# Optimization experiments

Hardware: AMD Instinct MI355X
Metric: run time of the kernel (lower is better)

Reference implementation:

```python
import jax, jax.numpy as jnp
import numpy as np

D_MODEL = 1024
N_HEADS = 16
D_HEAD = D_MODEL // N_HEADS
D_FF = 4096
THETA = 10000.0
EPS = 1e-5


def rmsnorm(x, g):
    xf = x.astype(jnp.float32)
    rms = jnp.sqrt(jnp.mean(xf * xf, axis=-1, keepdims=True) + EPS)
    return ((xf / rms) * g).astype(x.dtype)


def rope(x, pos):
    # x: (B, H, S, d_head); pos: (S,) int
    dk = x.shape[-1]
    inv_freq = 1.0 / (THETA ** (jnp.arange(0, dk, 2, dtype=jnp.float32) / dk))
    freqs = pos.astype(jnp.float32)[:, None] * inv_freq[None, :]  # (S, dk/2)
    cos, sin = jnp.cos(freqs), jnp.sin(freqs)
    xp = x.reshape(*x.shape[:-1], dk // 2, 2)
    xe, xo = xp[..., 0], xp[..., 1]
    re = xe * cos - xo * sin
    ro = xe * sin + xo * cos
    return jnp.stack([re, ro], axis=-1).reshape(x.shape)


def attention(x, pos, q_w, k_w, v_w, o_w):
    B, S, D = x.shape
    def heads(t):
        return t.reshape(B, S, N_HEADS, D_HEAD).transpose(0, 2, 1, 3)
    Q = heads(x @ q_w.T)
    K = heads(x @ k_w.T)
    V = heads(x @ v_w.T)
    Q = rope(Q, pos)
    K = rope(K, pos)
    scores = jnp.einsum('bhqd,bhkd->bhqk', Q, K) / jnp.sqrt(jnp.float32(D_HEAD))
    causal = jnp.tril(jnp.ones((S, S), dtype=bool))
    scores = jnp.where(causal[None, None], scores, -jnp.inf)
    attn = jax.nn.softmax(scores, axis=-1)
    H = jnp.einsum('bhqk,bhkd->bhqd', attn, V)
    H = H.transpose(0, 2, 1, 3).reshape(B, S, D)
    return H @ o_w.T


def swiglu(x, w1, w2, w3):
    a = x @ w1.T
    swish = a * jax.nn.sigmoid(a)
    gate = x @ w3.T
    return (swish * gate) @ w2.T


def setup_inputs() -> dict:
    key = jax.random.key(0)
    ks = jax.random.split(key, 8)
    B, S = 4, 2048
    std_ff = (2.0 / (D_MODEL + D_FF)) ** 0.5
    return {
        'x': jax.random.normal(ks[0], (B, S, D_MODEL), jnp.float32),
        'token_positions': jnp.arange(S, dtype=jnp.int32),
        'q_w': jax.random.truncated_normal(ks[1], -3, 3, (D_MODEL, D_MODEL), jnp.float32),
        'k_w': jax.random.truncated_normal(ks[2], -3, 3, (D_MODEL, D_MODEL), jnp.float32),
        'v_w': jax.random.truncated_normal(ks[3], -3, 3, (D_MODEL, D_MODEL), jnp.float32),
        'o_w': jax.random.truncated_normal(ks[4], -3, 3, (D_MODEL, D_MODEL), jnp.float32),
        'g1': jnp.ones((D_MODEL,), jnp.float32),
        'g2': jnp.ones((D_MODEL,), jnp.float32),
        'w1': jax.random.truncated_normal(ks[5], -3, 3, (D_FF, D_MODEL), jnp.float32) * std_ff,
        'w2': jax.random.truncated_normal(ks[6], -3, 3, (D_MODEL, D_FF), jnp.float32) * std_ff,
        'w3': jax.random.truncated_normal(ks[7], -3, 3, (D_FF, D_MODEL), jnp.float32) * std_ff,
    }


def reference(x, token_positions, q_w, k_w, v_w, o_w, g1, g2, w1, w2, w3):
    x_norm = rmsnorm(x, g1)
    O = x + attention(x_norm, token_positions, q_w, k_w, v_w, o_w)
    H = O + swiglu(rmsnorm(O, g2), w1, w2, w3)
    return H
```

## Files before the change

kernel.cpp:

```cpp
#include <hip/hip_runtime.h>
#include <stdint.h>


typedef short bf16x8 __attribute__((ext_vector_type(8)));
typedef float f32x4  __attribute__((ext_vector_type(4)));

#define DEV static __device__ __forceinline__

DEV float bf2f(uint32_t u) { uint32_t v = u << 16; float f; __builtin_memcpy(&f, &v, 4); return f; }
DEV uint16_t f2bf(float f) {
  uint32_t u; __builtin_memcpy(&u, &f, 4);
  u = (u + 0x7fffu + ((u >> 16) & 1u)) >> 16;
  return (uint16_t)u;
}

DEV void gl_lds16(const uint16_t* g, uint16_t* l) {
  __builtin_amdgcn_global_load_lds((const __attribute__((address_space(1))) uint32_t*)g,
                                   (__attribute__((address_space(3))) uint32_t*)l, 16, 0, 0);
}


__global__ __launch_bounds__(256) void cvt_bf16_k(const float* __restrict__ src,
                                                  uint16_t* __restrict__ dst, int n4) {
  const int t = blockIdx.x * 256 + threadIdx.x;
  if (t >= n4) return;
  const float4 v = ((const float4*)src)[t];
  ushort4 o; o.x = f2bf(v.x); o.y = f2bf(v.y); o.z = f2bf(v.z); o.w = f2bf(v.w);
  ((ushort4*)dst)[t] = o;
}

__global__ __launch_bounds__(256) void cvt_split_qk_k(const float* __restrict__ qw,
                                                      const float* __restrict__ kw,
                                                      uint16_t* __restrict__ hi,
                                                      uint16_t* __restrict__ lo) {
  const int t = blockIdx.x * 256 + threadIdx.x;
  const int row = t >> 8, c4 = t & 255;
  const float* src = (row < 1024) ? (qw + (size_t)row * 1024)
                                  : (kw + (size_t)(row - 1024) * 1024);
  const float4 v = ((const float4*)src)[c4];
  ushort4 h, l;
  h.x = f2bf(v.x); l.x = f2bf(v.x - bf2f(h.x));
  h.y = f2bf(v.y); l.y = f2bf(v.y - bf2f(h.y));
  h.z = f2bf(v.z); l.z = f2bf(v.z - bf2f(h.z));
  h.w = f2bf(v.w); l.w = f2bf(v.w - bf2f(h.w));
  ((ushort4*)hi)[t] = h; ((ushort4*)lo)[t] = l;
}


template <bool SPLIT>
__global__ __launch_bounds__(256) void rmsnorm_k(const float* __restrict__ xin,
                                                 const float* __restrict__ g,
                                                 uint16_t* __restrict__ hi,
                                                 uint16_t* __restrict__ lo) {
  const int row = blockIdx.x, t = threadIdx.x;
  const float4 v = ((const float4*)(xin + (size_t)row * 1024))[t];
  float ss = v.x * v.x + v.y * v.y + v.z * v.z + v.w * v.w;
#pragma unroll
  for (int m = 1; m < 64; m <<= 1) ss += __shfl_xor(ss, m);
  __shared__ float red[4];
  if ((t & 63) == 0) red[t >> 6] = ss;
  __syncthreads();
  const float rinv = rsqrtf((red[0] + red[1] + red[2] + red[3]) * (1.0f / 1024.0f) + 1e-5f);
  const float4 gv = ((const float4*)g)[t];
  float y[4] = { v.x * rinv * gv.x, v.y * rinv * gv.y, v.z * rinv * gv.z, v.w * rinv * gv.w };
  ushort4 h; h.x = f2bf(y[0]); h.y = f2bf(y[1]); h.z = f2bf(y[2]); h.w = f2bf(y[3]);
  ((ushort4*)(hi + (size_t)row * 1024))[t] = h;
  if constexpr (SPLIT) {
    ushort4 l;
    l.x = f2bf(y[0] - bf2f(h.x)); l.y = f2bf(y[1] - bf2f(h.y));
    l.z = f2bf(y[2] - bf2f(h.z)); l.w = f2bf(y[3] - bf2f(h.w));
    ((ushort4*)(lo + (size_t)row * 1024))[t] = l;
  }
}


template <int OUT>
__global__ __launch_bounds__(256) void gemm_bt_k(const uint16_t* __restrict__ A,
                                                 const uint16_t* __restrict__ B,
                                                 void* __restrict__ C,
                                                 const float* __restrict__ resid,
                                                 int N, int K) {
  __shared__ __align__(16) uint16_t As[128 * 64];
  __shared__ __align__(16) uint16_t Bs[128 * 64];
  const int t = threadIdx.x, w = t >> 6, lane = t & 63, m16 = lane & 15, quad = lane >> 4;
  const int wm = (w >> 1) * 64, wn = (w & 1) * 64;
  const int mBase = blockIdx.y * 128, nBase = blockIdx.x * 128;
  f32x4 acc[4][4];
  const f32x4 vz = {0.f, 0.f, 0.f, 0.f};
#pragma unroll
  for (int i = 0; i < 4; ++i)
#pragma unroll
    for (int j = 0; j < 4; ++j) acc[i][j] = vz;
  const int r_ = t >> 3, g_ = t & 7, sg = g_ ^ (r_ & 7);
  const uint16_t* ag = A + (size_t)(mBase + r_) * K + sg * 8;
  const uint16_t* bg = B + (size_t)(nBase + r_) * K + sg * 8;
  for (int k0 = 0; k0 < K; k0 += 64) {
#pragma unroll
    for (int it = 0; it < 4; ++it) {
      gl_lds16(ag + (size_t)(it * 32) * K + k0, As + it * 2048 + t * 8);
      gl_lds16(bg + (size_t)(it * 32) * K + k0, Bs + it * 2048 + t * 8);
    }
    __syncthreads();
#pragma unroll
    for (int ks = 0; ks < 2; ++ks) {
      bf16x8 af[4], bf4[4];
      const int cg = ks * 4 + quad;
#pragma unroll
      for (int i = 0; i < 4; ++i) {
        const int rA = wm + i * 16 + m16;
        af[i] = *(const bf16x8*)(As + rA * 64 + ((cg ^ (rA & 7)) * 8));
        const int rB = wn + i * 16 + m16;
        bf4[i] = *(const bf16x8*)(Bs + rB * 64 + ((cg ^ (rB & 7)) * 8));
      }
#pragma unroll
      for (int i = 0; i < 4; ++i)
#pragma unroll
        for (int j = 0; j < 4; ++j)
          acc[i][j] = __builtin_amdgcn_mfma_f32_16x16x32_bf16(af[i], bf4[j], acc[i][j], 0, 0, 0);
    }
    __syncthreads();
  }
#pragma unroll
  for (int i = 0; i < 4; ++i) {
    const int row0 = mBase + wm + i * 16 + quad * 4;
#pragma unroll
    for (int j = 0; j < 4; ++j) {
      const int col = nBase + wn + j * 16 + m16;
#pragma unroll
      for (int r = 0; r < 4; ++r) {
        const size_t idx = (size_t)(row0 + r) * N + col;
        const float v = acc[i][j][r];
        if constexpr (OUT == 1) ((float*)C)[idx] = v + resid[idx];
        else                    ((uint16_t*)C)[idx] = f2bf(v);
      }
    }
  }
}


__global__ __launch_bounds__(256) void gemm_bt_split_k(
    const uint16_t* __restrict__ Ahi, const uint16_t* __restrict__ Alo,
    const uint16_t* __restrict__ Bhi, const uint16_t* __restrict__ Blo,
    uint16_t* __restrict__ Chi, uint16_t* __restrict__ Clo, int N, int K) {
  __shared__ __align__(16) uint16_t Ah[128 * 32];
  __shared__ __align__(16) uint16_t Al[128 * 32];
  __shared__ __align__(16) uint16_t Bh[128 * 32];
  __shared__ __align__(16) uint16_t Bl[128 * 32];
  const int t = threadIdx.x, w = t >> 6, lane = t & 63, m16 = lane & 15, quad = lane >> 4;
  const int wm = (w >> 1) * 64, wn = (w & 1) * 64;
  const int mBase = blockIdx.y * 128, nBase = blockIdx.x * 128;
  f32x4 acc[4][4];
  const f32x4 vz = {0.f, 0.f, 0.f, 0.f};
#pragma unroll
  for (int i = 0; i < 4; ++i)
#pragma unroll
    for (int j = 0; j < 4; ++j) acc[i][j] = vz;
  const int r_ = t >> 2, g_ = t & 3, sg = g_ ^ (r_ & 3);
  const uint16_t* agh = Ahi + (size_t)(mBase + r_) * K + sg * 8;
  const uint16_t* agl = Alo + (size_t)(mBase + r_) * K + sg * 8;
  const uint16_t* bgh = Bhi + (size_t)(nBase + r_) * K + sg * 8;
  const uint16_t* bgl = Blo + (size_t)(nBase + r_) * K + sg * 8;
  for (int k0 = 0; k0 < K; k0 += 32) {
#pragma unroll
    for (int it = 0; it < 2; ++it) {
      gl_lds16(agh + (size_t)(it * 64) * K + k0, Ah + it * 2048 + t * 8);
      gl_lds16(agl + (size_t)(it * 64) * K + k0, Al + it * 2048 + t * 8);
      gl_lds16(bgh + (size_t)(it * 64) * K + k0, Bh + it * 2048 + t * 8);
      gl_lds16(bgl + (size_t)(it * 64) * K + k0, Bl + it * 2048 + t * 8);
    }
    __syncthreads();
    bf16x8 ah[4], al[4], bh4[4], bl4[4];
#pragma unroll
    for (int i = 0; i < 4; ++i) {
      const int rA = wm + i * 16 + m16;
      const int offA = rA * 32 + ((quad ^ (rA & 3)) * 8);
      ah[i] = *(const bf16x8*)(Ah + offA);
      al[i] = *(const bf16x8*)(Al + offA);
      const int rB = wn + i * 16 + m16;
      const int offB = rB * 32 + ((quad ^ (rB & 3)) * 8);
      bh4[i] = *(const bf16x8*)(Bh + offB);
      bl4[i] = *(const bf16x8*)(Bl + offB);
    }
#pragma unroll
    for (int i = 0; i < 4; ++i)
#pragma unroll
      for (int j = 0; j < 4; ++j) {
        acc[i][j] = __builtin_amdgcn_mfma_f32_16x16x32_bf16(ah[i], bh4[j], acc[i][j], 0, 0, 0);
        acc[i][j] = __builtin_amdgcn_mfma_f32_16x16x32_bf16(ah[i], bl4[j], acc[i][j], 0, 0, 0);
        acc[i][j] = __builtin_amdgcn_mfma_f32_16x16x32_bf16(al[i], bh4[j], acc[i][j], 0, 0, 0);
      }
    __syncthreads();
  }
#pragma unroll
  for (int i = 0; i < 4; ++i) {
    const int row0 = mBase + wm + i * 16 + quad * 4;
#pragma unroll
    for (int j = 0; j < 4; ++j) {
      const int col = nBase + wn + j * 16 + m16;
#pragma unroll
      for (int r = 0; r < 4; ++r) {
        const size_t idx = (size_t)(row0 + r) * N + col;
        const float v = acc[i][j][r];
        const uint16_t hh = f2bf(v);
        Chi[idx] = hh;
        Clo[idx] = f2bf(v - bf2f(hh));
      }
    }
  }
}


__global__ __launch_bounds__(256) void rope_k(uint16_t* __restrict__ qkh,
                                              uint16_t* __restrict__ qkl,
                                              const int* __restrict__ pos) {
  const int t = blockIdx.x * 256 + threadIdx.x;
  const int row = t >> 10, p = t & 1023;
  const int which = p >> 9, hp = p & 511, h = hp >> 5, d2 = hp & 31;
  const size_t idx = (size_t)row * 2048 + which * 1024 + h * 64 + d2 * 2;
  const uint32_t ph = *(const uint32_t*)(qkh + idx);
  const uint32_t pl = *(const uint32_t*)(qkl + idx);
  const float xe = bf2f(ph & 0xffffu) + bf2f(pl & 0xffffu);
  const float xo = bf2f(ph >> 16) + bf2f(pl >> 16);
  const float inv_freq = exp2f((float)d2 * -0.41524101186092029f);
  const float fr = (float)pos[row & 2047] * inv_freq;
  float sn, cs; sincosf(fr, &sn, &cs);
  const float re = xe * cs - xo * sn;
  const float ro = xe * sn + xo * cs;
  const uint16_t reh = f2bf(re), roh = f2bf(ro);
  const uint16_t rel = f2bf(re - bf2f(reh)), rol = f2bf(ro - bf2f(roh));
  *(uint32_t*)(qkh + idx) = (uint32_t)reh | ((uint32_t)roh << 16);
  *(uint32_t*)(qkl + idx) = (uint32_t)rel | ((uint32_t)rol << 16);
}


__global__ __launch_bounds__(256) void transpose_v_k(const uint16_t* __restrict__ V,
                                                     uint16_t* __restrict__ Vt) {
  __shared__ __align__(16) uint16_t tile[64][72];
  const int st = blockIdx.x, bh = blockIdx.y, b = bh >> 4, h = bh & 15;
  const int t = threadIdx.x;
  {
    const int sl = t >> 3, dg = t & 7;
#pragma unroll
    for (int it = 0; it < 2; ++it) {
      const int s = it * 32 + sl;
      const uint4 v = *(const uint4*)(V + (size_t)(b * 2048 + st * 64 + s) * 1024 + h * 64 + dg * 8);
      *(uint4*)(&tile[s][dg * 8]) = v;
    }
  }
  __syncthreads();
  {
    const int dl = t >> 3, sg2 = t & 7;
#pragma unroll
    for (int it = 0; it < 2; ++it) {
      const int d = it * 32 + dl;
      union { uint4 v; uint16_t u[8]; } pk;
#pragma unroll
      for (int r = 0; r < 8; ++r) pk.u[r] = tile[sg2 * 8 + r][d];
      *(uint4*)(Vt + (size_t)(bh * 64 + d) * 2048 + st * 64 + sg2 * 8) = pk.v;
    }
  }
}


__global__ __launch_bounds__(256) void flash_k(const uint16_t* __restrict__ Qh,
                                               const uint16_t* __restrict__ Ql,
                                               const uint16_t* __restrict__ Vt,
                                               uint16_t* __restrict__ Hout) {
  __shared__ __align__(16) uint16_t Kh[64 * 64];
  __shared__ __align__(16) uint16_t Kl[64 * 64];
  __shared__ __align__(16) uint16_t Vs[64 * 64];
  __shared__ __align__(16) uint16_t P[4][32 * 72];

  const int bh = blockIdx.y, b = bh >> 4, h = bh & 15;
  const int t = threadIdx.x, w = t >> 6, lane = t & 63, m16 = lane & 15, quad = lane >> 4;

  const int r_ = t >> 3, g_ = t & 7, sgx = g_ ^ (r_ & 7);
  const uint16_t* khg = Qh + (size_t)(b * 2048 + r_) * 2048 + 1024 + h * 64 + sgx * 8;
  const uint16_t* klg = Ql + (size_t)(b * 2048 + r_) * 2048 + 1024 + h * 64 + sgx * 8;
  const uint16_t* vtg = Vt + (size_t)(bh * 64 + r_) * 2048 + sgx * 8;

  for (int half = 0; half < 2; ++half) {
    const int qt = half ? (15 - (int)blockIdx.x) : (int)blockIdx.x;

    bf16x8 qh[2][2], ql[2][2];
#pragma unroll
    for (int i = 0; i < 2; ++i) {
      const int row = b * 2048 + qt * 128 + w * 32 + i * 16 + m16;
#pragma unroll
      for (int ks = 0; ks < 2; ++ks) {
        const size_t offq = (size_t)row * 2048 + h * 64 + ks * 32 + quad * 8;
        qh[i][ks] = *(const bf16x8*)(Qh + offq);
        ql[i][ks] = *(const bf16x8*)(Ql + offq);
      }
    }

    float mr[2][4], lr[2][4];
    f32x4 o[2][4];
    const f32x4 vz = {0.f, 0.f, 0.f, 0.f};
#pragma unroll
    for (int i = 0; i < 2; ++i)
#pragma unroll
      for (int r = 0; r < 4; ++r) { mr[i][r] = -1e30f; lr[i][r] = 0.f; }
#pragma unroll
    for (int i = 0; i < 2; ++i)
#pragma unroll
      for (int n = 0; n < 4; ++n) o[i][n] = vz;

    const int ktEnd = 2 * qt + 2;
    for (int kt = 0; kt < ktEnd; ++kt) {
#pragma unroll
      for (int it = 0; it < 2; ++it) {
        gl_lds16(khg + (size_t)(kt * 64 + it * 32) * 2048, Kh + it * 2048 + t * 8);
        gl_lds16(klg + (size_t)(kt * 64 + it * 32) * 2048, Kl + it * 2048 + t * 8);
        gl_lds16(vtg + (size_t)(it * 32) * 2048 + kt * 64, Vs + it * 2048 + t * 8);
      }
      __syncthreads();

      f32x4 sc[2][4];
#pragma unroll
      for (int i = 0; i < 2; ++i)
#pragma unroll
        for (int j = 0; j < 4; ++j) sc[i][j] = vz;
#pragma unroll
      for (int ks = 0; ks < 2; ++ks) {
        bf16x8 kfh[4], kfl[4];
        const int cg = ks * 4 + quad;
#pragma unroll
        for (int j = 0; j < 4; ++j) {
          const int rK = j * 16 + m16;
          const int offk = rK * 64 + ((cg ^ (rK & 7)) * 8);
          kfh[j] = *(const bf16x8*)(Kh + offk);
          kfl[j] = *(const bf16x8*)(Kl + offk);
        }
#pragma unroll
        for (int i = 0; i < 2; ++i)
#pragma unroll
          for (int j = 0; j < 4; ++j) {
            sc[i][j] = __builtin_amdgcn_mfma_f32_16x16x32_bf16(qh[i][ks], kfh[j], sc[i][j], 0, 0, 0);
            sc[i][j] = __builtin_amdgcn_mfma_f32_16x16x32_bf16(qh[i][ks], kfl[j], sc[i][j], 0, 0, 0);
            sc[i][j] = __builtin_amdgcn_mfma_f32_16x16x32_bf16(ql[i][ks], kfh[j], sc[i][j], 0, 0, 0);
          }
      }

#pragma unroll
      for (int i = 0; i < 2; ++i) {
#pragma unroll
        for (int r = 0; r < 4; ++r) {
          const int qg = qt * 128 + w * 32 + i * 16 + quad * 4 + r;
          float mx = -1e30f;
#pragma unroll
          for (int j = 0; j < 4; ++j) {
            float v = sc[i][j][r] * 0.125f;
            const int kg = kt * 64 + j * 16 + m16;
            if (kg > qg) v = -1e30f;
            sc[i][j][r] = v;
            mx = fmaxf(mx, v);
          }
#pragma unroll
          for (int m = 1; m < 16; m <<= 1) mx = fmaxf(mx, __shfl_xor(mx, m));
          const float mnew = fmaxf(mr[i][r], mx);
          const float alpha = __expf(mr[i][r] - mnew);
          mr[i][r] = mnew;
          float ls = 0.f;
#pragma unroll
          for (int j = 0; j < 4; ++j) {
            const float pv = __expf(sc[i][j][r] - mnew);
            sc[i][j][r] = pv;
            ls += pv;
          }
#pragma unroll
          for (int m = 1; m < 16; m <<= 1) ls += __shfl_xor(ls, m);
          lr[i][r] = lr[i][r] * alpha + ls;
#pragma unroll
          for (int n = 0; n < 4; ++n) o[i][n][r] *= alpha;
        }
#pragma unroll
        for (int j = 0; j < 4; ++j)
#pragma unroll
          for (int r = 0; r < 4; ++r)
            P[w][(i * 16 + quad * 4 + r) * 72 + j * 16 + m16] = f2bf(sc[i][j][r]);
      }
      __syncthreads();

#pragma unroll
      for (int ks2 = 0; ks2 < 2; ++ks2) {
        bf16x8 pf[2], vf[4];
#pragma unroll
        for (int i = 0; i < 2; ++i)
          pf[i] = *(const bf16x8*)(&P[w][(i * 16 + m16) * 72 + ks2 * 32 + quad * 8]);
        const int cg = ks2 * 4 + quad;
#pragma unroll
        for (int n = 0; n < 4; ++n) {
          const int rV = n * 16 + m16;
          vf[n] = *(const bf16x8*)(Vs + rV * 64 + ((cg ^ (rV & 7)) * 8));
        }
#pragma unroll
        for (int i = 0; i < 2; ++i)
#pragma unroll
          for (int n = 0; n < 4; ++n)
            o[i][n] = __builtin_amdgcn_mfma_f32_16x16x32_bf16(pf[i], vf[n], o[i][n], 0, 0, 0);
      }
      __syncthreads();
    }

#pragma unroll
    for (int i = 0; i < 2; ++i)
#pragma unroll
      for (int r = 0; r < 4; ++r) {
        const float inv = 1.f / lr[i][r];
        const size_t row = (size_t)(b * 2048 + qt * 128 + w * 32 + i * 16 + quad * 4 + r);
#pragma unroll
        for (int n = 0; n < 4; ++n)
          Hout[row * 1024 + h * 64 + n * 16 + m16] = f2bf(o[i][n][r] * inv);
      }
  }
}


__global__ __launch_bounds__(256) void swiglu_k(uint16_t* __restrict__ a,
                                                const uint16_t* __restrict__ g, int n8) {
  const int t = blockIdx.x * 256 + threadIdx.x;
  if (t >= n8) return;
  union { uint4 v; uint16_t u[8]; } av, gv, hv;
  av.v = ((const uint4*)a)[t];
  gv.v = ((const uint4*)g)[t];
#pragma unroll
  for (int e = 0; e < 8; ++e) {
    const float x = bf2f(av.u[e]);
    const float gg = bf2f(gv.u[e]);
    const float sw = x / (1.f + __expf(-x));
    hv.u[e] = f2bf(sw * gg);
  }
  ((uint4*)a)[t] = hv.v;
}


extern "C" void kernel_launch(void* const* d_in, const int* in_sizes, int n_in,
                              void* d_out, int out_size, void* d_ws, size_t ws_size,
                              hipStream_t stream) {
  (void)in_sizes; (void)n_in; (void)out_size; (void)ws_size;
  const float* x   = (const float*)d_in[0];
  const int*   pos = (const int*)  d_in[1];
  const float* q_w = (const float*)d_in[2];
  const float* k_w = (const float*)d_in[3];
  const float* v_w = (const float*)d_in[4];
  const float* o_w = (const float*)d_in[5];
  const float* g1  = (const float*)d_in[6];
  const float* g2  = (const float*)d_in[7];
  const float* w1  = (const float*)d_in[8];
  const float* w2  = (const float*)d_in[9];
  const float* w3  = (const float*)d_in[10];

  char* ws = (char*)d_ws;
  uint16_t* wqk_hi = (uint16_t*)(ws + 0);
  uint16_t* wqk_lo = (uint16_t*)(ws + 4194304);
  uint16_t* wv     = (uint16_t*)(ws + 8388608);
  uint16_t* wo     = (uint16_t*)(ws + 10485760);
  uint16_t* w1b    = (uint16_t*)(ws + 12582912);
  uint16_t* w3b    = (uint16_t*)(ws + 20971520);
  uint16_t* w2b    = (uint16_t*)(ws + 29360128);
  uint16_t* xn_hi  = (uint16_t*)(ws + 37748736);
  uint16_t* xn_lo  = (uint16_t*)(ws + 54525952);
  uint16_t* vbuf   = (uint16_t*)(ws + 71303168);
  uint16_t* vt     = (uint16_t*)(ws + 88080384);
  uint16_t* qk_hi  = (uint16_t*)(ws + 104857600);
  uint16_t* qk_lo  = (uint16_t*)(ws + 138412032);
  uint16_t* hbuf   = (uint16_t*)(ws + 171966464);
  float*    ores   = (float*)   (ws + 188743680);
  uint16_t* on2    = (uint16_t*)(ws + 222298112);
  uint16_t* abuf   = (uint16_t*)(ws + 104857600);
  uint16_t* gbuf   = (uint16_t*)(ws + 37748736);

  cvt_split_qk_k<<<2048, 256, 0, stream>>>(q_w, k_w, wqk_hi, wqk_lo);
  cvt_bf16_k<<<1024, 256, 0, stream>>>(v_w, wv, 262144);
  cvt_bf16_k<<<1024, 256, 0, stream>>>(o_w, wo, 262144);
  cvt_bf16_k<<<4096, 256, 0, stream>>>(w1, w1b, 1048576);
  cvt_bf16_k<<<4096, 256, 0, stream>>>(w3, w3b, 1048576);
  cvt_bf16_k<<<4096, 256, 0, stream>>>(w2, w2b, 1048576);

  rmsnorm_k<true><<<8192, 256, 0, stream>>>(x, g1, xn_hi, xn_lo);

  gemm_bt_split_k<<<dim3(16, 64), 256, 0, stream>>>(xn_hi, xn_lo, wqk_hi, wqk_lo,
                                                    qk_hi, qk_lo, 2048, 1024);
  gemm_bt_k<0><<<dim3(8, 64), 256, 0, stream>>>(xn_hi, wv, (void*)vbuf, nullptr, 1024, 1024);

  rope_k<<<32768, 256, 0, stream>>>(qk_hi, qk_lo, pos);
  transpose_v_k<<<dim3(32, 64), 256, 0, stream>>>(vbuf, vt);

  flash_k<<<dim3(8, 64), 256, 0, stream>>>(qk_hi, qk_lo, vt, hbuf);

  gemm_bt_k<1><<<dim3(8, 64), 256, 0, stream>>>(hbuf, wo, (void*)ores, x, 1024, 1024);

  rmsnorm_k<false><<<8192, 256, 0, stream>>>(ores, g2, on2, nullptr);

  gemm_bt_k<0><<<dim3(32, 64), 256, 0, stream>>>(on2, w1b, (void*)abuf, nullptr, 4096, 1024);
  gemm_bt_k<0><<<dim3(32, 64), 256, 0, stream>>>(on2, w3b, (void*)gbuf, nullptr, 4096, 1024);
  swiglu_k<<<16384, 256, 0, stream>>>(abuf, gbuf, 4194304);

  gemm_bt_k<1><<<dim3(8, 64), 256, 0, stream>>>(abuf, w2b, d_out, ores, 1024, 4096);
}
```

Measured before the change: 872.1 us.

## Double-buffer K/V tiles in flash attention with async prefetch and exp2 softmax

Doubles the K/V LDS buffers so the next tile's global-to-LDS loads are issued before computing on the current tile. The loop now waits with explicit vmcnt counts and raw barriers instead of two __syncthreads per iteration. It also removes the per-wave P sync, folds the 1/8 scale and log2(e) into an exp2 FMA, skips causal masking on tiles that are fully below the diagonal, and raises wave priority around the MFMA blocks. This aims to hide load latency and trim VALU work, at the cost of doubled LDS use (lower occupancy) and fragile hand-tuned waitcnt logic.

```diff
diff --git a/kernel.cpp b/kernel.cpp
--- a/kernel.cpp
+++ b/kernel.cpp
@@ -266,9 +266,9 @@
                                                const uint16_t* __restrict__ Ql,
                                                const uint16_t* __restrict__ Vt,
                                                uint16_t* __restrict__ Hout) {
-  __shared__ __align__(16) uint16_t Kh[64 * 64];
-  __shared__ __align__(16) uint16_t Kl[64 * 64];
-  __shared__ __align__(16) uint16_t Vs[64 * 64];
+  __shared__ __align__(16) uint16_t Kh[2][64 * 64];
+  __shared__ __align__(16) uint16_t Kl[2][64 * 64];
+  __shared__ __align__(16) uint16_t Vs[2][64 * 64];
   __shared__ __align__(16) uint16_t P[4][32 * 72];
 
   const int bh = blockIdx.y, b = bh >> 4, h = bh & 15;
@@ -279,6 +279,8 @@
   const uint16_t* klg = Ql + (size_t)(b * 2048 + r_) * 2048 + 1024 + h * 64 + sgx * 8;
   const uint16_t* vtg = Vt + (size_t)(bh * 64 + r_) * 2048 + sgx * 8;
 
+  const float nscl = 0.18033688011112042f;
+
   for (int half = 0; half < 2; ++half) {
     const int qt = half ? (15 - (int)blockIdx.x) : (int)blockIdx.x;
 
@@ -293,6 +295,20 @@
         ql[i][ks] = *(const bf16x8*)(Ql + offq);
       }
     }
+#pragma unroll
+    for (int i = 0; i < 2; ++i)
+#pragma unroll
+      for (int ks = 0; ks < 2; ++ks)
+        asm volatile("" : "+v"(qh[i][ks]), "+v"(ql[i][ks]));
+
+    const int ktEnd = 2 * qt + 2;
+
+#pragma unroll
+    for (int it = 0; it < 2; ++it) {
+      gl_lds16(khg + (size_t)(it * 32) * 2048, &Kh[0][it * 2048 + t * 8]);
+      gl_lds16(klg + (size_t)(it * 32) * 2048, &Kl[0][it * 2048 + t * 8]);
+      gl_lds16(vtg + (size_t)(it * 32) * 2048, &Vs[0][it * 2048 + t * 8]);
+    }
 
     float mr[2][4], lr[2][4];
     f32x4 o[2][4];
@@ -306,15 +322,24 @@
 #pragma unroll
       for (int n = 0; n < 4; ++n) o[i][n] = vz;
 
-    const int ktEnd = 2 * qt + 2;
     for (int kt = 0; kt < ktEnd; ++kt) {
-#pragma unroll
-      for (int it = 0; it < 2; ++it) {
-        gl_lds16(khg + (size_t)(kt * 64 + it * 32) * 2048, Kh + it * 2048 + t * 8);
-        gl_lds16(klg + (size_t)(kt * 64 + it * 32) * 2048, Kl + it * 2048 + t * 8);
-        gl_lds16(vtg + (size_t)(it * 32) * 2048 + kt * 64, Vs + it * 2048 + t * 8);
-      }
-      __syncthreads();
+      const int cur = kt & 1, nxt = cur ^ 1;
+      __builtin_amdgcn_s_barrier();
+      __builtin_amdgcn_sched_barrier(0);
+      if (kt + 1 < ktEnd) {
+        const int kn = kt + 1;
+#pragma unroll
+        for (int it = 0; it < 2; ++it) {
+          gl_lds16(khg + (size_t)(kn * 64 + it * 32) * 2048, &Kh[nxt][it * 2048 + t * 8]);
+          gl_lds16(klg + (size_t)(kn * 64 + it * 32) * 2048, &Kl[nxt][it * 2048 + t * 8]);
+          gl_lds16(vtg + (size_t)(it * 32) * 2048 + kn * 64, &Vs[nxt][it * 2048 + t * 8]);
+        }
+        asm volatile("s_waitcnt vmcnt(6)" ::: "memory");
+      } else {
+        asm volatile("s_waitcnt vmcnt(0)" ::: "memory");
+      }
+      __builtin_amdgcn_s_barrier();
+      __builtin_amdgcn_sched_barrier(0);
 
       f32x4 sc[2][4];
 #pragma unroll
@@ -329,9 +354,10 @@
         for (int j = 0; j < 4; ++j) {
           const int rK = j * 16 + m16;
           const int offk = rK * 64 + ((cg ^ (rK & 7)) * 8);
-          kfh[j] = *(const bf16x8*)(Kh + offk);
-          kfl[j] = *(const bf16x8*)(Kl + offk);
+          kfh[j] = *(const bf16x8*)(&Kh[cur][offk]);
+          kfl[j] = *(const bf16x8*)(&Kl[cur][offk]);
         }
+        __builtin_amdgcn_s_setprio(1);
 #pragma unroll
         for (int i = 0; i < 2; ++i)
 #pragma unroll
@@ -340,31 +366,39 @@
             sc[i][j] = __builtin_amdgcn_mfma_f32_16x16x32_bf16(qh[i][ks], kfl[j], sc[i][j], 0, 0, 0);
             sc[i][j] = __builtin_amdgcn_mfma_f32_16x16x32_bf16(ql[i][ks], kfh[j], sc[i][j], 0, 0, 0);
           }
+        __builtin_amdgcn_s_setprio(0);
       }
 
 #pragma unroll
       for (int i = 0; i < 2; ++i) {
+        const bool needMask = (kt * 64 + 63) > (qt * 128 + w * 32 + i * 16);
 #pragma unroll
         for (int r = 0; r < 4; ++r) {
-          const int qg = qt * 128 + w * 32 + i * 16 + quad * 4 + r;
           float mx = -1e30f;
-#pragma unroll
-          for (int j = 0; j < 4; ++j) {
-            float v = sc[i][j][r] * 0.125f;
-            const int kg = kt * 64 + j * 16 + m16;
-            if (kg > qg) v = -1e30f;
-            sc[i][j][r] = v;
-            mx = fmaxf(mx, v);
+          if (needMask) {
+            const int qg = qt * 128 + w * 32 + i * 16 + quad * 4 + r;
+#pragma unroll
+            for (int j = 0; j < 4; ++j) {
+              float v = sc[i][j][r];
+              const int kg = kt * 64 + j * 16 + m16;
+              if (kg > qg) v = -1e30f;
+              sc[i][j][r] = v;
+              mx = fmaxf(mx, v);
+            }
+          } else {
+#pragma unroll
+            for (int j = 0; j < 4; ++j) mx = fmaxf(mx, sc[i][j][r]);
           }
 #pragma unroll
           for (int m = 1; m < 16; m <<= 1) mx = fmaxf(mx, __shfl_xor(mx, m));
           const float mnew = fmaxf(mr[i][r], mx);
-          const float alpha = __expf(mr[i][r] - mnew);
+          const float alpha = __builtin_amdgcn_exp2f((mr[i][r] - mnew) * nscl);
           mr[i][r] = mnew;
+          const float nm = mnew * nscl;
           float ls = 0.f;
 #pragma unroll
           for (int j = 0; j < 4; ++j) {
-            const float pv = __expf(sc[i][j][r] - mnew);
+            const float pv = __builtin_amdgcn_exp2f(__builtin_fmaf(sc[i][j][r], nscl, -nm));
             sc[i][j][r] = pv;
             ls += pv;
           }
@@ -380,7 +414,6 @@
           for (int r = 0; r < 4; ++r)
             P[w][(i * 16 + quad * 4 + r) * 72 + j * 16 + m16] = f2bf(sc[i][j][r]);
       }
-      __syncthreads();
 
 #pragma unroll
       for (int ks2 = 0; ks2 < 2; ++ks2) {
@@ -392,15 +425,16 @@
 #pragma unroll
         for (int n = 0; n < 4; ++n) {
           const int rV = n * 16 + m16;
-          vf[n] = *(const bf16x8*)(Vs + rV * 64 + ((cg ^ (rV & 7)) * 8));
+          vf[n] = *(const bf16x8*)(&Vs[cur][rV * 64 + ((cg ^ (rV & 7)) * 8)]);
         }
+        __builtin_amdgcn_s_setprio(1);
 #pragma unroll
         for (int i = 0; i < 2; ++i)
 #pragma unroll
           for (int n = 0; n < 4; ++n)
             o[i][n] = __builtin_amdgcn_mfma_f32_16x16x32_bf16(pf[i], vf[n], o[i][n], 0, 0, 0);
-      }
-      __syncthreads();
+        __builtin_amdgcn_s_setprio(0);
+      }
     }
 
 #pragma unroll
@@ -413,6 +447,7 @@
         for (int n = 0; n < 4; ++n)
           Hout[row * 1024 + h * 64 + n * 16 + m16] = f2bf(o[i][n][r] * inv);
       }
+    __syncthreads();
   }
 }
 
```

Result: faster. 846.6 us (-2.9%).
